# Kernel tuning notes

Measured on AMD Instinct MI355X. Metric: run time of the kernel, lower is better.

## Reference

```python
import jax, jax.numpy as jnp
import numpy as np


def _conv(x, w, stride, padding):
    # x: NCHW, w: OIHW
    return jax.lax.conv_general_dilated(
        x, w,
        window_strides=(stride, stride),
        padding=[(padding, padding), (padding, padding)],
        dimension_numbers=("NCHW", "OIHW", "NCHW"),
    )


def setup_inputs() -> dict:
    key = jax.random.key(0)
    ks = jax.random.split(key, 7)
    N, C_in, H0, W0 = 64, 128, 56, 56
    C_out = 256
    x = jax.random.normal(ks[0], (N, C_in, H0, W0), dtype=jnp.float32)
    w1 = jax.random.normal(ks[1], (C_out, C_in, 3, 3), dtype=jnp.float32) * 0.05
    b1 = jax.random.normal(ks[2], (C_out,), dtype=jnp.float32) * 0.05
    w2 = jax.random.normal(ks[3], (C_out, C_out, 3, 3), dtype=jnp.float32) * 0.05
    b2 = jax.random.normal(ks[4], (C_out,), dtype=jnp.float32) * 0.05
    wds = jax.random.normal(ks[5], (C_out, C_in, 1, 1), dtype=jnp.float32) * 0.05
    bds = jax.random.normal(ks[6], (C_out,), dtype=jnp.float32) * 0.05
    return {"x": x, "w1": w1, "b1": b1, "w2": w2, "b2": b2, "wds": wds, "bds": bds}


def reference(x, w1, b1, w2, b2, wds, bds):
    stride = 2
    # conv1 (BN folded) + bias + ReLU -> act: (N, C_out, H1, W1)
    act = jax.nn.relu(_conv(x, w1, stride, 1) + b1[None, :, None, None])
    # fused: conv2 3x3 (pad 1) + b2 + 1x1 strided downsample of x + bds, then ReLU
    main = _conv(act, w2, 1, 1) + b2[None, :, None, None]
    shortcut = _conv(x, wds, stride, 0) + bds[None, :, None, None]
    return jax.nn.relu(main + shortcut)
```

## Files before the change

### kernel.cpp

```cpp
#include <hip/hip_runtime.h>
#include <hip/hip_bf16.h>

typedef short short8 __attribute__((ext_vector_type(8)));
typedef float floatx4 __attribute__((ext_vector_type(4)));
typedef __hip_bfloat16 bf16;

#define GLB(p) ((const __attribute__((address_space(1))) void*)(p))
#define LDSP(p) ((__attribute__((address_space(3))) void*)(p))

__device__ __forceinline__ void gload16(const bf16* g, char* l) {
    __builtin_amdgcn_global_load_lds(GLB(g), LDSP(l), 16, 0, 0);
}

#define VMCNT(n) asm volatile("s_waitcnt vmcnt(" #n ")" ::: "memory")
#define LGKM0()  asm volatile("s_waitcnt lgkmcnt(0)" ::: "memory")
#define BAR()    __builtin_amdgcn_s_barrier()

#define XPAD_BYTES   (64u*58*58*128*2)
#define ACTPAD_BYTES (64u*30*30*256*2)
#define OFF_XPAD   0
#define OFF_ACTPAD (XPAD_BYTES)
#define OFF_W1T    (OFF_ACTPAD + ACTPAD_BYTES)
#define OFF_W2T    (OFF_W1T + 1152u*256*2)
#define OFF_WDST   (OFF_W2T + 2304u*256*2)

__global__ void wtrans_kernel(const float* __restrict__ w1, const float* __restrict__ w2,
                              const float* __restrict__ wds,
                              bf16* __restrict__ w1t, bf16* __restrict__ w2t,
                              bf16* __restrict__ wdst) {
    int i = blockIdx.x * 256 + threadIdx.x;
    if (i < 256 * 1152) {
        int oc = i / 1152, k = i % 1152, tap = k >> 7, ic = k & 127;
        w1t[i] = __float2bfloat16(w1[(oc * 128 + ic) * 9 + tap]);
    }
    if (i < 256 * 2304) {
        int oc = i / 2304, k = i % 2304, tap = k >> 8, ic = k & 255;
        w2t[i] = __float2bfloat16(w2[(oc * 256 + ic) * 9 + tap]);
    }
    if (i < 256 * 128) {
        wdst[i] = __float2bfloat16(wds[i]);
    }
}

__global__ void halo_zero_kernel(bf16* __restrict__ xpad, bf16* __restrict__ actpad) {
    int i = blockIdx.x * 256 + threadIdx.x;
    uint4 z; z.x = z.y = z.z = z.w = 0;
    const int n0 = 64 * 2 * 58 * 16;
    const int n1 = n0 + 64 * 56 * 2 * 16;
    const int n2 = n1 + 64 * 2 * 30 * 32;
    const int n3 = n2 + 64 * 28 * 2 * 32;
    if (i < n0) {
        int g = i & 15, w = (i >> 4) % 58, q = (i >> 4) / 58;
        int n = q >> 1, h = (q & 1) ? 57 : 0;
        *(uint4*)(xpad + ((size_t)((n * 58 + h) * 58 + w)) * 128 + g * 8) = z;
    } else if (i < n1) {
        int j = i - n0;
        int g = j & 15, q = j >> 4;
        int w = (q & 1) ? 57 : 0, h = (q >> 1) % 56 + 1, n = (q >> 1) / 56;
        *(uint4*)(xpad + ((size_t)((n * 58 + h) * 58 + w)) * 128 + g * 8) = z;
    } else if (i < n2) {
        int j = i - n1;
        int g = j & 31, w = (j >> 5) % 30, q = (j >> 5) / 30;
        int n = q >> 1, h = (q & 1) ? 29 : 0;
        *(uint4*)(actpad + ((size_t)((n * 30 + h) * 30 + w)) * 256 + g * 8) = z;
    } else if (i < n3) {
        int j = i - n2;
        int g = j & 31, q = j >> 5;
        int w = (q & 1) ? 29 : 0, h = (q >> 1) % 28 + 1, n = (q >> 1) / 28;
        *(uint4*)(actpad + ((size_t)((n * 30 + h) * 30 + w)) * 256 + g * 8) = z;
    }
}

__global__ void xpad_kernel(const float* __restrict__ x, bf16* __restrict__ xpad) {
    int bid = blockIdx.x;
    int n = bid / 56, h = bid % 56;
    __shared__ float tile[128 * 57];
    const float* src = x + ((size_t)n * 128) * 3136 + h * 56;
    for (int e = threadIdx.x; e < 128 * 56; e += 256) {
        int c = e / 56, w = e % 56;
        tile[c * 57 + w] = src[(size_t)c * 3136 + w];
    }
    __syncthreads();
    bf16* dst = xpad + ((size_t)(n * 58 + h + 1) * 58 + 1) * 128;
    for (int e = threadIdx.x; e < 56 * 16; e += 256) {
        int w = e / 16, g = e % 16;
        union { bf16 b[8]; uint4 v; } o;
        #pragma unroll
        for (int j = 0; j < 8; ++j)
            o.b[j] = __float2bfloat16(tile[(g * 8 + j) * 57 + w]);
        *(uint4*)(dst + (size_t)w * 128 + g * 8) = o.v;
    }
}

__global__ __launch_bounds__(512, 2) void conv1_kernel(
    const bf16* __restrict__ xpad, const bf16* __restrict__ w1t,
    const float* __restrict__ b1, bf16* __restrict__ actpad)
{
    __shared__ __align__(16) char lds[131072];
    const int t = threadIdx.x;
    const int m0 = blockIdx.x * 256;

    const int unit = t & 3, srow = t >> 2;
    int xb[2], wb[2];
    #pragma unroll
    for (int r = 0; r < 2; ++r) {
        int m = m0 + r * 128 + srow;
        int n = m / 784, pix = m % 784, oh = pix / 28, ow = pix % 28;
        xb[r] = ((n * 58 + 2 * oh) * 58 + 2 * ow) * 128 + unit * 8;
        wb[r] = (r * 128 + srow) * 1152 + unit * 8;
    }
    char* const ldsA = lds + t * 16;
    char* const ldsB = lds + 16384 + t * 16;

    auto STAGE_A = [&](int kt, int slot) {
        int tap = kt >> 2, chunk = kt & 3;
        int kh = (tap * 11) >> 5, kw = tap - kh * 3;
        int toff = (kh * 58 + kw) * 128 + chunk * 32;
        gload16(xpad + xb[0] + toff, ldsA + slot * 32768);
        gload16(xpad + xb[1] + toff, ldsA + slot * 32768 + 8192);
    };
    auto STAGE_B = [&](int kt, int slot) {
        gload16(w1t + wb[0] + kt * 32, ldsB + slot * 32768);
        gload16(w1t + wb[1] + kt * 32, ldsB + slot * 32768 + 8192);
    };

    const int lane = t & 63, wid = t >> 6;
    const int wm = (wid >> 2) << 7, woc = (wid & 3) << 6;
    const int lr = lane & 15, kg = lane >> 4;
    int aoff[8], boff[4];
    #pragma unroll
    for (int f = 0; f < 8; ++f) aoff[f] = (wm + f * 16 + lr) * 64 + kg * 16;
    #pragma unroll
    for (int g = 0; g < 4; ++g) boff[g] = 16384 + (woc + g * 16 + lr) * 64 + kg * 16;

    floatx4 acc[8][4];
    #pragma unroll
    for (int a = 0; a < 8; ++a)
        #pragma unroll
        for (int b = 0; b < 4; ++b) acc[a][b] = (floatx4){0.f, 0.f, 0.f, 0.f};

    STAGE_A(0, 0); STAGE_B(0, 0);
    STAGE_A(1, 1); STAGE_B(1, 1);
    STAGE_A(2, 2); STAGE_B(2, 2);
    VMCNT(8); BAR();

    #pragma unroll 4
    for (int kt = 0; kt < 36; ++kt) {
        const int cs = kt & 3;
        const char* base = lds + (cs << 15);
        short8 wfr[4];
        #pragma unroll
        for (int g = 0; g < 4; ++g) wfr[g] = *(const short8*)(base + boff[g]);
        {
            short8 afr[4];
            #pragma unroll
            for (int f = 0; f < 4; ++f) afr[f] = *(const short8*)(base + aoff[f]);
            if (kt + 3 < 36) STAGE_A(kt + 3, (kt + 3) & 3);
            BAR(); LGKM0();
            __builtin_amdgcn_s_setprio(1);
            #pragma unroll
            for (int f = 0; f < 4; ++f)
                #pragma unroll
                for (int fo = 0; fo < 4; ++fo)
                    acc[f][fo] = __builtin_amdgcn_mfma_f32_16x16x32_bf16(afr[f], wfr[fo], acc[f][fo], 0, 0, 0);
            __builtin_amdgcn_s_setprio(0);
            BAR();
        }
        {
            short8 afr[4];
            #pragma unroll
            for (int f = 0; f < 4; ++f) afr[f] = *(const short8*)(base + aoff[4 + f]);
            if (kt + 3 < 36) STAGE_B(kt + 3, (kt + 3) & 3);
            BAR(); LGKM0();
            __builtin_amdgcn_s_setprio(1);
            #pragma unroll
            for (int f = 0; f < 4; ++f)
                #pragma unroll
                for (int fo = 0; fo < 4; ++fo)
                    acc[4 + f][fo] = __builtin_amdgcn_mfma_f32_16x16x32_bf16(afr[f], wfr[fo], acc[4 + f][fo], 0, 0, 0);
            __builtin_amdgcn_s_setprio(0);
            int rem = 35 - kt;
            if (rem >= 3) { VMCNT(8); }
            else if (rem == 2) { VMCNT(4); }
            else if (rem == 1) { VMCNT(0); }
            BAR();
        }
    }

    #pragma unroll
    for (int fm = 0; fm < 8; ++fm) {
        #pragma unroll
        for (int rg = 0; rg < 4; ++rg) {
            int m = m0 + wm + fm * 16 + (kg << 2) + rg;
            int n = m / 784, pix = m % 784;
            int oh = pix / 28, ow = pix % 28;
            bf16* dst = actpad + ((size_t)(n * 30 + oh + 1) * 30 + (ow + 1)) * 256;
            #pragma unroll
            for (int fo = 0; fo < 4; ++fo) {
                int oc = woc + fo * 16 + lr;
                float v = acc[fm][fo][rg] + b1[oc];
                dst[oc] = __float2bfloat16(fmaxf(v, 0.0f));
            }
        }
    }
}

__global__ __launch_bounds__(512, 2) void conv2_kernel(
    const bf16* __restrict__ actpad, const bf16* __restrict__ xpad,
    const bf16* __restrict__ w2t, const bf16* __restrict__ wdst,
    const float* __restrict__ b2, const float* __restrict__ bds,
    float* __restrict__ out)
{
    __shared__ __align__(16) char lds[131072];
    const int t = threadIdx.x;
    const int m0 = blockIdx.x * 256;

    const int unit = t & 3, srow = t >> 2;
    int ab[2], xb[2], wb[2], db[2];
    #pragma unroll
    for (int r = 0; r < 2; ++r) {
        int m = m0 + r * 128 + srow;
        int n = m / 784, pix = m % 784, oh = pix / 28, ow = pix % 28;
        ab[r] = ((n * 30 + oh) * 30 + ow) * 256 + unit * 8;
        xb[r] = ((n * 58 + 2 * oh + 1) * 58 + (2 * ow + 1)) * 128 + unit * 8;
        wb[r] = (r * 128 + srow) * 2304 + unit * 8;
        db[r] = (r * 128 + srow) * 128 + unit * 8;
    }
    char* const ldsA = lds + t * 16;
    char* const ldsB = lds + 16384 + t * 16;

    auto STAGE_A = [&](int kt, int slot) {
        if (kt < 72) {
            int tap = kt >> 3, chunk = kt & 7;
            int kh = (tap * 11) >> 5, kw = tap - kh * 3;
            int toff = (kh * 30 + kw) * 256 + chunk * 32;
            gload16(actpad + ab[0] + toff, ldsA + slot * 32768);
            gload16(actpad + ab[1] + toff, ldsA + slot * 32768 + 8192);
        } else {
            int chunk = kt - 72;
            gload16(xpad + xb[0] + chunk * 32, ldsA + slot * 32768);
            gload16(xpad + xb[1] + chunk * 32, ldsA + slot * 32768 + 8192);
        }
    };
    auto STAGE_B = [&](int kt, int slot) {
        if (kt < 72) {
            gload16(w2t + wb[0] + kt * 32, ldsB + slot * 32768);
            gload16(w2t + wb[1] + kt * 32, ldsB + slot * 32768 + 8192);
        } else {
            int chunk = kt - 72;
            gload16(wdst + db[0] + chunk * 32, ldsB + slot * 32768);
            gload16(wdst + db[1] + chunk * 32, ldsB + slot * 32768 + 8192);
        }
    };

    const int lane = t & 63, wid = t >> 6;
    const int wm = (wid >> 2) << 7, woc = (wid & 3) << 6;
    const int lr = lane & 15, kg = lane >> 4;
    int aoff[8], boff[4];
    #pragma unroll
    for (int f = 0; f < 8; ++f) aoff[f] = (wm + f * 16 + lr) * 64 + kg * 16;
    #pragma unroll
    for (int g = 0; g < 4; ++g) boff[g] = 16384 + (woc + g * 16 + lr) * 64 + kg * 16;

    floatx4 acc[8][4];
    #pragma unroll
    for (int a = 0; a < 8; ++a)
        #pragma unroll
        for (int b = 0; b < 4; ++b) acc[a][b] = (floatx4){0.f, 0.f, 0.f, 0.f};

    STAGE_A(0, 0); STAGE_B(0, 0);
    STAGE_A(1, 1); STAGE_B(1, 1);
    STAGE_A(2, 2); STAGE_B(2, 2);
    VMCNT(8); BAR();

    #pragma unroll 4
    for (int kt = 0; kt < 76; ++kt) {
        const int cs = kt & 3;
        const char* base = lds + (cs << 15);
        short8 wfr[4];
        #pragma unroll
        for (int g = 0; g < 4; ++g) wfr[g] = *(const short8*)(base + boff[g]);
        {
            short8 afr[4];
            #pragma unroll
            for (int f = 0; f < 4; ++f) afr[f] = *(const short8*)(base + aoff[f]);
            if (kt + 3 < 76) STAGE_A(kt + 3, (kt + 3) & 3);
            BAR(); LGKM0();
            __builtin_amdgcn_s_setprio(1);
            #pragma unroll
            for (int f = 0; f < 4; ++f)
                #pragma unroll
                for (int fo = 0; fo < 4; ++fo)
                    acc[f][fo] = __builtin_amdgcn_mfma_f32_16x16x32_bf16(wfr[fo], afr[f], acc[f][fo], 0, 0, 0);
            __builtin_amdgcn_s_setprio(0);
            BAR();
        }
        {
            short8 afr[4];
            #pragma unroll
            for (int f = 0; f < 4; ++f) afr[f] = *(const short8*)(base + aoff[4 + f]);
            if (kt + 3 < 76) STAGE_B(kt + 3, (kt + 3) & 3);
            BAR(); LGKM0();
            __builtin_amdgcn_s_setprio(1);
            #pragma unroll
            for (int f = 0; f < 4; ++f)
                #pragma unroll
                for (int fo = 0; fo < 4; ++fo)
                    acc[4 + f][fo] = __builtin_amdgcn_mfma_f32_16x16x32_bf16(wfr[fo], afr[f], acc[4 + f][fo], 0, 0, 0);
            __builtin_amdgcn_s_setprio(0);
            int rem = 75 - kt;
            if (rem >= 3) { VMCNT(8); }
            else if (rem == 2) { VMCNT(4); }
            else if (rem == 1) { VMCNT(0); }
            BAR();
        }
    }

    #pragma unroll
    for (int fm = 0; fm < 8; ++fm) {
        int mcol = m0 + wm + fm * 16 + lr;
        int n = mcol / 784, pix = mcol % 784;
        float* obase = out + (size_t)n * 200704 + pix;
        #pragma unroll
        for (int fo = 0; fo < 4; ++fo) {
            int ocb = woc + fo * 16 + (kg << 2);
            #pragma unroll
            for (int rg = 0; rg < 4; ++rg) {
                int oc = ocb + rg;
                float v = acc[fm][fo][rg] + b2[oc] + bds[oc];
                obase[(size_t)oc * 784] = fmaxf(v, 0.0f);
            }
        }
    }
}

extern "C" void kernel_launch(void* const* d_in, const int* in_sizes, int n_in,
                              void* d_out, int out_size, void* d_ws, size_t ws_size,
                              hipStream_t stream) {
    const float* x   = (const float*)d_in[0];
    const float* w1  = (const float*)d_in[1];
    const float* b1  = (const float*)d_in[2];
    const float* w2  = (const float*)d_in[3];
    const float* b2  = (const float*)d_in[4];
    const float* wds = (const float*)d_in[5];
    const float* bds = (const float*)d_in[6];
    float* out = (float*)d_out;

    char* ws = (char*)d_ws;
    bf16* xpad   = (bf16*)(ws + OFF_XPAD);
    bf16* actpad = (bf16*)(ws + OFF_ACTPAD);
    bf16* w1t    = (bf16*)(ws + OFF_W1T);
    bf16* w2t    = (bf16*)(ws + OFF_W2T);
    bf16* wdst   = (bf16*)(ws + OFF_WDST);

    halo_zero_kernel<<<1840, 256, 0, stream>>>(xpad, actpad);
    wtrans_kernel<<<2304, 256, 0, stream>>>(w1, w2, wds, w1t, w2t, wdst);
    xpad_kernel<<<64 * 56, 256, 0, stream>>>(x, xpad);
    conv1_kernel<<<196, 512, 0, stream>>>(xpad, w1t, b1, actpad);
    conv2_kernel<<<196, 512, 0, stream>>>(actpad, xpad, w2t, wdst, b2, bds, out);
}
```

Before: 321.6 us.

## XOR-swizzle LDS k-chunks and hoist all fragment reads ahead of barriers

Both conv kernels now XOR-swizzle the 16-byte k-chunk position by row, applied both when staging global data into LDS and when computing fragment read offsets, to cut LDS bank conflicts on the short8 fragment reads. The main loop also reads all A fragments (both halves) up front. It drops one barrier pair and the explicit lgkmcnt waits, so the second staging overlaps with the MFMAs. In exchange the kernels hold more fragment registers and rely on the compiler to insert LDS waits correctly.

```diff
diff --git a/kernel.cpp b/kernel.cpp
--- a/kernel.cpp
+++ b/kernel.cpp
@@ -13,7 +13,6 @@
 }
 
 #define VMCNT(n) asm volatile("s_waitcnt vmcnt(" #n ")" ::: "memory")
-#define LGKM0()  asm volatile("s_waitcnt lgkmcnt(0)" ::: "memory")
 #define BAR()    __builtin_amdgcn_s_barrier()
 
 #define XPAD_BYTES   (64u*58*58*128*2)
@@ -100,14 +99,15 @@
     const int t = threadIdx.x;
     const int m0 = blockIdx.x * 256;
 
-    const int unit = t & 3, srow = t >> 2;
+    const int srow = t >> 2;
+    const int su = (t & 3) ^ ((srow >> 1) & 3);
     int xb[2], wb[2];
     #pragma unroll
     for (int r = 0; r < 2; ++r) {
         int m = m0 + r * 128 + srow;
         int n = m / 784, pix = m % 784, oh = pix / 28, ow = pix % 28;
-        xb[r] = ((n * 58 + 2 * oh) * 58 + 2 * ow) * 128 + unit * 8;
-        wb[r] = (r * 128 + srow) * 1152 + unit * 8;
+        xb[r] = ((n * 58 + 2 * oh) * 58 + 2 * ow) * 128 + su * 8;
+        wb[r] = (r * 128 + srow) * 1152 + su * 8;
     }
     char* const ldsA = lds + t * 16;
     char* const ldsB = lds + 16384 + t * 16;
@@ -127,11 +127,12 @@
     const int lane = t & 63, wid = t >> 6;
     const int wm = (wid >> 2) << 7, woc = (wid & 3) << 6;
     const int lr = lane & 15, kg = lane >> 4;
+    const int ks = (kg ^ ((lr >> 1) & 3)) << 4;
     int aoff[8], boff[4];
     #pragma unroll
-    for (int f = 0; f < 8; ++f) aoff[f] = (wm + f * 16 + lr) * 64 + kg * 16;
-    #pragma unroll
-    for (int g = 0; g < 4; ++g) boff[g] = 16384 + (woc + g * 16 + lr) * 64 + kg * 16;
+    for (int f = 0; f < 8; ++f) aoff[f] = (wm + f * 16 + lr) * 64 + ks;
+    #pragma unroll
+    for (int g = 0; g < 4; ++g) boff[g] = 16384 + (woc + g * 16 + lr) * 64 + ks;
 
     floatx4 acc[8][4];
     #pragma unroll
@@ -148,43 +149,36 @@
     for (int kt = 0; kt < 36; ++kt) {
         const int cs = kt & 3;
         const char* base = lds + (cs << 15);
-        short8 wfr[4];
+        short8 wfr[4], afrA[4], afrB[4];
         #pragma unroll
         for (int g = 0; g < 4; ++g) wfr[g] = *(const short8*)(base + boff[g]);
-        {
-            short8 afr[4];
-            #pragma unroll
-            for (int f = 0; f < 4; ++f) afr[f] = *(const short8*)(base + aoff[f]);
-            if (kt + 3 < 36) STAGE_A(kt + 3, (kt + 3) & 3);
-            BAR(); LGKM0();
-            __builtin_amdgcn_s_setprio(1);
-            #pragma unroll
-            for (int f = 0; f < 4; ++f)
-                #pragma unroll
-                for (int fo = 0; fo < 4; ++fo)
-                    acc[f][fo] = __builtin_amdgcn_mfma_f32_16x16x32_bf16(afr[f], wfr[fo], acc[f][fo], 0, 0, 0);
-            __builtin_amdgcn_s_setprio(0);
-            BAR();
-        }
-        {
-            short8 afr[4];
-            #pragma unroll
-            for (int f = 0; f < 4; ++f) afr[f] = *(const short8*)(base + aoff[4 + f]);
-            if (kt + 3 < 36) STAGE_B(kt + 3, (kt + 3) & 3);
-            BAR(); LGKM0();
-            __builtin_amdgcn_s_setprio(1);
-            #pragma unroll
-            for (int f = 0; f < 4; ++f)
-                #pragma unroll
-                for (int fo = 0; fo < 4; ++fo)
-                    acc[4 + f][fo] = __builtin_amdgcn_mfma_f32_16x16x32_bf16(afr[f], wfr[fo], acc[4 + f][fo], 0, 0, 0);
-            __builtin_amdgcn_s_setprio(0);
-            int rem = 35 - kt;
-            if (rem >= 3) { VMCNT(8); }
-            else if (rem == 2) { VMCNT(4); }
-            else if (rem == 1) { VMCNT(0); }
-            BAR();
-        }
+        #pragma unroll
+        for (int f = 0; f < 4; ++f) afrA[f] = *(const short8*)(base + aoff[f]);
+        #pragma unroll
+        for (int f = 0; f < 4; ++f) afrB[f] = *(const short8*)(base + aoff[4 + f]);
+        if (kt + 3 < 36) STAGE_A(kt + 3, (kt + 3) & 3);
+        BAR();
+        __builtin_amdgcn_s_setprio(1);
+        #pragma unroll
+        for (int f = 0; f < 4; ++f)
+            #pragma unroll
+            for (int fo = 0; fo < 4; ++fo)
+                acc[f][fo] = __builtin_amdgcn_mfma_f32_16x16x32_bf16(afrA[f], wfr[fo], acc[f][fo], 0, 0, 0);
+        __builtin_amdgcn_s_setprio(0);
+        BAR();
+        if (kt + 3 < 36) STAGE_B(kt + 3, (kt + 3) & 3);
+        __builtin_amdgcn_s_setprio(1);
+        #pragma unroll
+        for (int f = 0; f < 4; ++f)
+            #pragma unroll
+            for (int fo = 0; fo < 4; ++fo)
+                acc[4 + f][fo] = __builtin_amdgcn_mfma_f32_16x16x32_bf16(afrB[f], wfr[fo], acc[4 + f][fo], 0, 0, 0);
+        __builtin_amdgcn_s_setprio(0);
+        int rem = 35 - kt;
+        if (rem >= 3) { VMCNT(8); }
+        else if (rem == 2) { VMCNT(4); }
+        else if (rem == 1) { VMCNT(0); }
+        BAR();
     }
 
     #pragma unroll
@@ -215,16 +209,17 @@
     const int t = threadIdx.x;
     const int m0 = blockIdx.x * 256;
 
-    const int unit = t & 3, srow = t >> 2;
+    const int srow = t >> 2;
+    const int su = (t & 3) ^ ((srow >> 1) & 3);
     int ab[2], xb[2], wb[2], db[2];
     #pragma unroll
     for (int r = 0; r < 2; ++r) {
         int m = m0 + r * 128 + srow;
         int n = m / 784, pix = m % 784, oh = pix / 28, ow = pix % 28;
-        ab[r] = ((n * 30 + oh) * 30 + ow) * 256 + unit * 8;
-        xb[r] = ((n * 58 + 2 * oh + 1) * 58 + (2 * ow + 1)) * 128 + unit * 8;
-        wb[r] = (r * 128 + srow) * 2304 + unit * 8;
-        db[r] = (r * 128 + srow) * 128 + unit * 8;
+        ab[r] = ((n * 30 + oh) * 30 + ow) * 256 + su * 8;
+        xb[r] = ((n * 58 + 2 * oh + 1) * 58 + (2 * ow + 1)) * 128 + su * 8;
+        wb[r] = (r * 128 + srow) * 2304 + su * 8;
+        db[r] = (r * 128 + srow) * 128 + su * 8;
     }
     char* const ldsA = lds + t * 16;
     char* const ldsB = lds + 16384 + t * 16;
@@ -256,11 +251,12 @@
     const int lane = t & 63, wid = t >> 6;
     const int wm = (wid >> 2) << 7, woc = (wid & 3) << 6;
     const int lr = lane & 15, kg = lane >> 4;
+    const int ks = (kg ^ ((lr >> 1) & 3)) << 4;
     int aoff[8], boff[4];
     #pragma unroll
-    for (int f = 0; f < 8; ++f) aoff[f] = (wm + f * 16 + lr) * 64 + kg * 16;
-    #pragma unroll
-    for (int g = 0; g < 4; ++g) boff[g] = 16384 + (woc + g * 16 + lr) * 64 + kg * 16;
+    for (int f = 0; f < 8; ++f) aoff[f] = (wm + f * 16 + lr) * 64 + ks;
+    #pragma unroll
+    for (int g = 0; g < 4; ++g) boff[g] = 16384 + (woc + g * 16 + lr) * 64 + ks;
 
     floatx4 acc[8][4];
     #pragma unroll
@@ -277,43 +273,36 @@
     for (int kt = 0; kt < 76; ++kt) {
         const int cs = kt & 3;
         const char* base = lds + (cs << 15);
-        short8 wfr[4];
+        short8 wfr[4], afrA[4], afrB[4];
         #pragma unroll
         for (int g = 0; g < 4; ++g) wfr[g] = *(const short8*)(base + boff[g]);
-        {
-            short8 afr[4];
-            #pragma unroll
-            for (int f = 0; f < 4; ++f) afr[f] = *(const short8*)(base + aoff[f]);
-            if (kt + 3 < 76) STAGE_A(kt + 3, (kt + 3) & 3);
-            BAR(); LGKM0();
-            __builtin_amdgcn_s_setprio(1);
-            #pragma unroll
-            for (int f = 0; f < 4; ++f)
-                #pragma unroll
-                for (int fo = 0; fo < 4; ++fo)
-                    acc[f][fo] = __builtin_amdgcn_mfma_f32_16x16x32_bf16(wfr[fo], afr[f], acc[f][fo], 0, 0, 0);
-            __builtin_amdgcn_s_setprio(0);
-            BAR();
-        }
-        {
-            short8 afr[4];
-            #pragma unroll
-            for (int f = 0; f < 4; ++f) afr[f] = *(const short8*)(base + aoff[4 + f]);
-            if (kt + 3 < 76) STAGE_B(kt + 3, (kt + 3) & 3);
-            BAR(); LGKM0();
-            __builtin_amdgcn_s_setprio(1);
-            #pragma unroll
-            for (int f = 0; f < 4; ++f)
-                #pragma unroll
-                for (int fo = 0; fo < 4; ++fo)
-                    acc[4 + f][fo] = __builtin_amdgcn_mfma_f32_16x16x32_bf16(wfr[fo], afr[f], acc[4 + f][fo], 0, 0, 0);
-            __builtin_amdgcn_s_setprio(0);
-            int rem = 75 - kt;
-            if (rem >= 3) { VMCNT(8); }
-            else if (rem == 2) { VMCNT(4); }
-            else if (rem == 1) { VMCNT(0); }
-            BAR();
-        }
+        #pragma unroll
+        for (int f = 0; f < 4; ++f) afrA[f] = *(const short8*)(base + aoff[f]);
+        #pragma unroll
+        for (int f = 0; f < 4; ++f) afrB[f] = *(const short8*)(base + aoff[4 + f]);
+        if (kt + 3 < 76) STAGE_A(kt + 3, (kt + 3) & 3);
+        BAR();
+        __builtin_amdgcn_s_setprio(1);
+        #pragma unroll
+        for (int f = 0; f < 4; ++f)
+            #pragma unroll
+            for (int fo = 0; fo < 4; ++fo)
+                acc[f][fo] = __builtin_amdgcn_mfma_f32_16x16x32_bf16(wfr[fo], afrA[f], acc[f][fo], 0, 0, 0);
+        __builtin_amdgcn_s_setprio(0);
+        BAR();
+        if (kt + 3 < 76) STAGE_B(kt + 3, (kt + 3) & 3);
+        __builtin_amdgcn_s_setprio(1);
+        #pragma unroll
+        for (int f = 0; f < 4; ++f)
+            #pragma unroll
+            for (int fo = 0; fo < 4; ++fo)
+                acc[4 + f][fo] = __builtin_amdgcn_mfma_f32_16x16x32_bf16(wfr[fo], afrB[f], acc[4 + f][fo], 0, 0, 0);
+        __builtin_amdgcn_s_setprio(0);
+        int rem = 75 - kt;
+        if (rem >= 3) { VMCNT(8); }
+        else if (rem == 2) { VMCNT(4); }
+        else if (rem == 1) { VMCNT(0); }
+        BAR();
     }
 
     #pragma unroll
```

Result: no change. 316.1 us (-1.7%).
